# Optimization experiments

Hardware: AMD Instinct MI355X
Metric: run time of the kernel (lower is better)

Reference implementation:

```python
import jax, jax.numpy as jnp
import numpy as np

B, S, D, H = 4, 2048, 1024, 16
HD = D // H


def setup_inputs() -> dict:
    key = jax.random.key(0)
    ks = jax.random.split(key, 6)
    scale = 1.0 / np.sqrt(D)
    return {
        'x': jax.random.normal(ks[0], (B, S, D), dtype=jnp.float32),
        'wq': jax.random.normal(ks[1], (D, D), dtype=jnp.float32) * scale,
        'wk': jax.random.normal(ks[2], (D, D), dtype=jnp.float32) * scale,
        'wv': jax.random.normal(ks[3], (D, D), dtype=jnp.float32) * scale,
        'wo': jax.random.normal(ks[4], (D, D), dtype=jnp.float32) * scale,
        'wo_b': jnp.zeros((D,), dtype=jnp.float32),
    }


def reference(x, wq, wk, wv, wo, wo_b):
    b, s, _ = x.shape
    # Linear projections (torch Linear: x @ W.T), reshape to [b, h, s, hd]
    def proj(w):
        return jnp.einsum('bsd,ed->bse', x, w).reshape(b, s, H, HD).transpose(0, 2, 1, 3)
    q, k, v = proj(wq), proj(wk), proj(wv)
    scores = jnp.einsum('bhqd,bhkd->bhqk', q, k)  # [b,h,s,s]
    causal = jnp.triu(jnp.ones((s, s), dtype=bool), k=1)
    scores = jnp.where(causal, -jnp.inf, scores)
    attn = jax.nn.softmax(scores / np.sqrt(HD), axis=-1)
    ctx = jnp.einsum('bhqk,bhkd->bhqd', attn, v)  # [b,h,s,hd]
    ctx = ctx.transpose(0, 2, 1, 3).reshape(b, s, D)
    return jnp.einsum('bsd,ed->bse', ctx, wo) + wo_b
```

## Files before the change

### kernel.cpp

```cpp
#include <hip/hip_runtime.h>

#define SB 4
#define SS 2048
#define SD 1024
#define SH 16
#define SHD 64
#define SM (SB * SS)

typedef __bf16 bf16x8 __attribute__((ext_vector_type(8)));
typedef float f32x4 __attribute__((ext_vector_type(4)));

static __device__ __forceinline__ unsigned short f2bf(float x) {
    unsigned int u = __builtin_bit_cast(unsigned int, x);
    u += 0x7fffu + ((u >> 16) & 1u);
    return (unsigned short)(u >> 16);
}

static __device__ __forceinline__ float fast_exp2(float x) {
#if __has_builtin(__builtin_amdgcn_exp2f)
    return __builtin_amdgcn_exp2f(x);
#else
    return exp2f(x);
#endif
}

static __device__ __forceinline__ unsigned int pkhi(float a, float b) {
    return __builtin_amdgcn_perm(__builtin_bit_cast(unsigned int, a),
                                 __builtin_bit_cast(unsigned int, b), 0x07060302u);
}

typedef __attribute__((address_space(1))) void GV;
typedef __attribute__((address_space(3))) void LV;

static __device__ __forceinline__ void async16(const void* g, void* l) {
    __builtin_amdgcn_global_load_lds((GV*)g, (LV*)l, 16, 0, 0);
}

#define QSCALE 0.18033688011112042f

__global__ __launch_bounds__(256) void cast_all(
    const float* __restrict__ x,  const float* __restrict__ wq,
    const float* __restrict__ wk, const float* __restrict__ wv,
    const float* __restrict__ wo,
    unsigned short* __restrict__ xb, unsigned short* __restrict__ wqkv,
    unsigned short* __restrict__ wo16) {
    int i = blockIdx.x * 256 + threadIdx.x;
    const float4* src;
    ushort4* dst;
    if (i < 2097152) {
        src = reinterpret_cast<const float4*>(x) + i;
        dst = reinterpret_cast<ushort4*>(xb) + i;
    } else {
        int j = i - 2097152;
        int which = j >> 18;
        int r = j & 262143;
        const float* ws_[4] = {wq, wk, wv, wo};
        src = reinterpret_cast<const float4*>(ws_[which]) + r;
        dst = (which < 3 ? reinterpret_cast<ushort4*>(wqkv) + which * 262144
                         : reinterpret_cast<ushort4*>(wo16)) + r;
    }
    float4 v = *src;
    ushort4 o;
    o.x = f2bf(v.x); o.y = f2bf(v.y); o.z = f2bf(v.z); o.w = f2bf(v.w);
    *dst = o;
}

__device__ __forceinline__ void gemm128_mainloop(
    const unsigned short* __restrict__ A,
    const unsigned short* __restrict__ Bt,
    int Kdim, int tileM, int tileN, int tid,
    unsigned short* As, unsigned short* Bs,
    f32x4 (&acc)[4][4]) {

    const int lane = tid & 63;
    const int quad = lane >> 4;
    const int col0 = lane & 15;
    const int wr = tid >> 7;
    const int wc = (tid >> 6) & 1;

    const int srow = tid >> 2;
    const int schunk = (tid & 3) * 8;
    const unsigned short* Ab = A + (size_t)(tileM + srow) * Kdim + schunk;
    const unsigned short* Bb = Bt + (size_t)(tileN + srow) * Kdim + schunk;
    char* AsB = (char*)As + tid * 16;
    char* BsB = (char*)Bs + tid * 16;
    const size_t rowskip = (size_t)64 * Kdim;

    for (int k0 = 0; k0 < Kdim; k0 += 32) {
        __syncthreads();
        async16(Ab + k0, AsB);
        async16(Ab + k0 + rowskip, AsB + 4096);
        async16(Bb + k0, BsB);
        async16(Bb + k0 + rowskip, BsB + 4096);
        __syncthreads();

        bf16x8 af[4], bfr[4];
#pragma unroll
        for (int rt = 0; rt < 4; ++rt)
            af[rt] = *reinterpret_cast<const bf16x8*>(
                As + (wr * 64 + rt * 16 + col0) * 32 + quad * 8);
#pragma unroll
        for (int ct = 0; ct < 4; ++ct)
            bfr[ct] = *reinterpret_cast<const bf16x8*>(
                Bs + (wc * 64 + ct * 16 + col0) * 32 + quad * 8);
#pragma unroll
        for (int rt = 0; rt < 4; ++rt)
#pragma unroll
            for (int ct = 0; ct < 4; ++ct)
                acc[rt][ct] = __builtin_amdgcn_mfma_f32_16x16x32_bf16(
                    af[rt], bfr[ct], acc[rt][ct], 0, 0, 0);
    }
}

__global__ __launch_bounds__(256) void gemm_qkv(
    const unsigned short* __restrict__ xb,
    const unsigned short* __restrict__ wqkv,
    unsigned short* __restrict__ Qd,
    unsigned short* __restrict__ Kd,
    unsigned short* __restrict__ Vtd) {

    __shared__ __align__(16) unsigned short As[128 * 32];
    __shared__ __align__(16) unsigned short Bs[128 * 32];
    const int tid = threadIdx.x;
    const int tileN = blockIdx.x * 128;
    const int tileM = blockIdx.y * 128;

    f32x4 acc[4][4];
    const f32x4 z = {0.f, 0.f, 0.f, 0.f};
#pragma unroll
    for (int i = 0; i < 4; ++i)
#pragma unroll
        for (int j = 0; j < 4; ++j) acc[i][j] = z;

    gemm128_mainloop(xb, wqkv, SD, tileM, tileN, tid, As, Bs, acc);

    const int lane = tid & 63, quad = lane >> 4, col0 = lane & 15;
    const int wr = tid >> 7, wc = (tid >> 6) & 1;

#pragma unroll
    for (int ct = 0; ct < 4; ++ct) {
        int n0 = tileN + wc * 64 + ct * 16;
        int which = n0 >> 10;
        int e0 = n0 & 1023;
        int h = e0 >> 6;
        int hd = (e0 & 63) + col0;
#pragma unroll
        for (int rt = 0; rt < 4; ++rt) {
            int m0 = tileM + wr * 64 + rt * 16 + quad * 4;
            int bb = m0 >> 11;
            int s0 = m0 & 2047;
            int bh = bb * SH + h;
            if (which == 0) {
                int base = (bh * SS + s0) * SHD + hd;
#pragma unroll
                for (int r = 0; r < 4; ++r)
                    Qd[base + r * SHD] = f2bf(acc[rt][ct][r] * QSCALE);
            } else if (which == 1) {
                int base = (bh * SS + s0) * SHD + hd;
#pragma unroll
                for (int r = 0; r < 4; ++r)
                    Kd[base + r * SHD] = f2bf(acc[rt][ct][r]);
            } else {
                int base = (bh * SHD + hd) * SS + s0;
                ushort4 pk;
                pk.x = f2bf(acc[rt][ct][0]);
                pk.y = f2bf(acc[rt][ct][1]);
                pk.z = f2bf(acc[rt][ct][2]);
                pk.w = f2bf(acc[rt][ct][3]);
                *reinterpret_cast<ushort4*>(Vtd + base) = pk;
            }
        }
    }
}

__global__ __launch_bounds__(256) void gemm_out(
    const unsigned short* __restrict__ ctx,
    const unsigned short* __restrict__ wo16,
    const float* __restrict__ wb,
    float* __restrict__ out) {

    __shared__ __align__(16) unsigned short As[128 * 32];
    __shared__ __align__(16) unsigned short Bs[128 * 32];
    const int tid = threadIdx.x;
    const int tileN = blockIdx.x * 128;
    const int tileM = blockIdx.y * 128;

    f32x4 acc[4][4];
    const f32x4 z = {0.f, 0.f, 0.f, 0.f};
#pragma unroll
    for (int i = 0; i < 4; ++i)
#pragma unroll
        for (int j = 0; j < 4; ++j) acc[i][j] = z;

    gemm128_mainloop(ctx, wo16, SD, tileM, tileN, tid, As, Bs, acc);

    const int lane = tid & 63, quad = lane >> 4, col0 = lane & 15;
    const int wr = tid >> 7, wc = (tid >> 6) & 1;

#pragma unroll
    for (int ct = 0; ct < 4; ++ct) {
        int n = tileN + wc * 64 + ct * 16 + col0;
        float bias = wb[n];
#pragma unroll
        for (int rt = 0; rt < 4; ++rt) {
            int m0 = tileM + wr * 64 + rt * 16 + quad * 4;
#pragma unroll
            for (int r = 0; r < 4; ++r)
                out[(size_t)(m0 + r) * SD + n] = acc[rt][ct][r] + bias;
        }
    }
}

#define PSTR 72

__device__ __forceinline__ void attn_pass(
    const unsigned short* __restrict__ Qg,
    const unsigned short* __restrict__ Kg,
    const unsigned short* __restrict__ Vtg,
    unsigned short* __restrict__ ctx,
    size_t base, int b, int h, int jj,
    int tid, int w, int quad, int col0,
    unsigned short* Ks0, unsigned short* Ks1,
    unsigned short* Vs0, unsigned short* Vs1,
    unsigned short* Psw, const bf16x8& ones) {

    const int q0 = jj * 128 + w * 32;

    bf16x8 bq[2][2];
#pragma unroll
    for (int g = 0; g < 2; ++g)
#pragma unroll
        for (int ks = 0; ks < 2; ++ks)
            bq[g][ks] = *reinterpret_cast<const bf16x8*>(
                Qg + base + (size_t)(q0 + g * 16 + col0) * SHD + ks * 32 + quad * 8);

    f32x4 ot[2][4], lacc[2];
    const f32x4 z = {0.f, 0.f, 0.f, 0.f};
#pragma unroll
    for (int g = 0; g < 2; ++g) {
        lacc[g] = z;
#pragma unroll
        for (int ct = 0; ct < 4; ++ct) ot[g][ct] = z;
    }

    const int srow0 = tid >> 3;
    const int scs = tid & 7;

    unsigned short* KsB[2] = {Ks0, Ks1};
    unsigned short* VsB[2] = {Vs0, Vs1};

    const int nkt = 2 * jj + 2;

    __syncthreads();
#pragma unroll
    for (int j = 0; j < 2; ++j) {
        int row = j * 32 + srow0;
        int chunk = scs ^ (row & 7);
        int slot16 = (j * 256 + tid) * 16;
        async16(Kg + base + (size_t)row * SHD + chunk * 8, (char*)Ks0 + slot16);
        async16(Vtg + base + (size_t)row * SS + chunk * 8, (char*)Vs0 + slot16);
    }

    for (int kt = 0; kt < nkt; ++kt) {
        const int kb = kt * 64;
        __syncthreads();

        if (kt + 1 < nkt) {
            const int kb1 = kb + 64;
            unsigned short* Kn = KsB[(kt + 1) & 1];
            unsigned short* Vn = VsB[(kt + 1) & 1];
#pragma unroll
            for (int j = 0; j < 2; ++j) {
                int row = j * 32 + srow0;
                int chunk = scs ^ (row & 7);
                int slot16 = (j * 256 + tid) * 16;
                async16(Kg + base + (size_t)(kb1 + row) * SHD + chunk * 8,
                        (char*)Kn + slot16);
                async16(Vtg + base + (size_t)row * SS + kb1 + chunk * 8,
                        (char*)Vn + slot16);
            }
        }

        if (kb > q0 + 31) continue;

        const unsigned short* Kc = KsB[kt & 1];
        const unsigned short* Vc = VsB[kt & 1];

        bf16x8 ak[4][2];
#pragma unroll
        for (int rt = 0; rt < 4; ++rt)
#pragma unroll
            for (int ks = 0; ks < 2; ++ks)
                ak[rt][ks] = *reinterpret_cast<const bf16x8*>(
                    &Kc[(rt * 16 + col0) * 64 + ((ks * 4 + quad) ^ (col0 & 7)) * 8]);

        f32x4 sc[2][4];
#pragma unroll
        for (int g = 0; g < 2; ++g)
#pragma unroll
            for (int rt = 0; rt < 4; ++rt) sc[g][rt] = z;
#pragma unroll
        for (int rt = 0; rt < 4; ++rt)
#pragma unroll
            for (int g = 0; g < 2; ++g) {
                sc[g][rt] = __builtin_amdgcn_mfma_f32_16x16x32_bf16(
                    ak[rt][0], bq[g][0], sc[g][rt], 0, 0, 0);
                sc[g][rt] = __builtin_amdgcn_mfma_f32_16x16x32_bf16(
                    ak[rt][1], bq[g][1], sc[g][rt], 0, 0, 0);
            }

        if (kb + 63 > q0) {
#pragma unroll
            for (int g = 0; g < 2; ++g) {
                int q = q0 + g * 16 + col0;
#pragma unroll
                for (int rt = 0; rt < 4; ++rt)
#pragma unroll
                    for (int r = 0; r < 4; ++r) {
                        int key = kb + rt * 16 + quad * 4 + r;
                        if (key > q) sc[g][rt][r] = -3.0e38f;
                    }
            }
        }

#pragma unroll
        for (int g = 0; g < 2; ++g)
#pragma unroll
            for (int rt = 0; rt < 4; ++rt)
#pragma unroll
                for (int r = 0; r < 4; ++r)
                    sc[g][rt][r] = fast_exp2(sc[g][rt][r]);

#pragma unroll
        for (int g = 0; g < 2; ++g) {
            unsigned short* Pw = Psw + g * 16 * PSTR;
#pragma unroll
            for (int rt = 0; rt < 4; ++rt) {
                uint2 pk;
                pk.x = pkhi(sc[g][rt][1], sc[g][rt][0]);
                pk.y = pkhi(sc[g][rt][3], sc[g][rt][2]);
                *reinterpret_cast<uint2*>(&Pw[col0 * PSTR + rt * 16 + quad * 4]) = pk;
            }
        }

#pragma unroll
        for (int ks = 0; ks < 2; ++ks) {
            bf16x8 bp[2];
#pragma unroll
            for (int g = 0; g < 2; ++g) {
                bp[g] = *reinterpret_cast<const bf16x8*>(
                    &Psw[g * 16 * PSTR + col0 * PSTR + ks * 32 + quad * 8]);
                lacc[g] = __builtin_amdgcn_mfma_f32_16x16x32_bf16(
                    ones, bp[g], lacc[g], 0, 0, 0);
            }
#pragma unroll
            for (int ct = 0; ct < 4; ++ct) {
                bf16x8 av = *reinterpret_cast<const bf16x8*>(
                    &Vc[(ct * 16 + col0) * 64 + ((ks * 4 + quad) ^ (col0 & 7)) * 8]);
#pragma unroll
                for (int g = 0; g < 2; ++g)
                    ot[g][ct] = __builtin_amdgcn_mfma_f32_16x16x32_bf16(
                        av, bp[g], ot[g][ct], 0, 0, 0);
            }
        }
    }

#pragma unroll
    for (int g = 0; g < 2; ++g) {
        float inv = 1.0f / lacc[g][0];
        int q = q0 + g * 16 + col0;
        size_t obase = ((size_t)b * SS + q) * SD + h * SHD;
#pragma unroll
        for (int ct = 0; ct < 4; ++ct) {
            uint2 pk;
            pk.x = pkhi(ot[g][ct][1] * inv, ot[g][ct][0] * inv);
            pk.y = pkhi(ot[g][ct][3] * inv, ot[g][ct][2] * inv);
            *reinterpret_cast<uint2*>(ctx + obase + ct * 16 + quad * 4) = pk;
        }
    }
}

__global__ __launch_bounds__(256) void attn_kernel(
    const unsigned short* __restrict__ Qg,
    const unsigned short* __restrict__ Kg,
    const unsigned short* __restrict__ Vtg,
    unsigned short* __restrict__ ctx) {

    __shared__ __align__(16) unsigned short Ks0[64 * 64];
    __shared__ __align__(16) unsigned short Ks1[64 * 64];
    __shared__ __align__(16) unsigned short Vs0[64 * 64];
    __shared__ __align__(16) unsigned short Vs1[64 * 64];
    __shared__ __align__(16) unsigned short Ps[8 * 16 * PSTR];

    const int tid = threadIdx.x;
    const int w = tid >> 6;
    const int lane = tid & 63;
    const int quad = lane >> 4;
    const int col0 = lane & 15;
    const int bh = blockIdx.y;
    const int b = bh >> 4;
    const int h = bh & 15;
    const size_t base = (size_t)bh * (SS * SHD);
    unsigned short* Psw = Ps + w * 2 * 16 * PSTR;

    bf16x8 ones;
#pragma unroll
    for (int i = 0; i < 8; ++i) ones[i] = (__bf16)1.0f;

    attn_pass(Qg, Kg, Vtg, ctx, base, b, h, blockIdx.x,
              tid, w, quad, col0, Ks0, Ks1, Vs0, Vs1, Psw, ones);
    attn_pass(Qg, Kg, Vtg, ctx, base, b, h, 15 - blockIdx.x,
              tid, w, quad, col0, Ks0, Ks1, Vs0, Vs1, Psw, ones);
}

extern "C" void kernel_launch(void* const* d_in, const int* in_sizes, int n_in,
                              void* d_out, int out_size, void* d_ws, size_t ws_size,
                              hipStream_t stream) {
    const float* x  = (const float*)d_in[0];
    const float* wq = (const float*)d_in[1];
    const float* wk = (const float*)d_in[2];
    const float* wv = (const float*)d_in[3];
    const float* wo = (const float*)d_in[4];
    const float* wb = (const float*)d_in[5];
    float* out = (float*)d_out;

    char* ws = (char*)d_ws;
    unsigned short* xb   = (unsigned short*)(ws + 0);
    unsigned short* wqkv = (unsigned short*)(ws + 16777216);
    unsigned short* q    = (unsigned short*)(ws + 23068672);
    unsigned short* k    = (unsigned short*)(ws + 39845888);
    unsigned short* vt   = (unsigned short*)(ws + 56623104);
    unsigned short* ctx  = (unsigned short*)(ws + 73400320);
    unsigned short* wo16 = (unsigned short*)(ws + 90177536);

    cast_all<<<12288, 256, 0, stream>>>(x, wq, wk, wv, wo, xb, wqkv, wo16);

    gemm_qkv<<<dim3(3 * SD / 128, SM / 128), 256, 0, stream>>>(xb, wqkv, q, k, vt);

    attn_kernel<<<dim3(8, SB * SH), 256, 0, stream>>>(q, k, vt, ctx);

    gemm_out<<<dim3(SD / 128, SM / 128), 256, 0, stream>>>(ctx, wo16, wb, out);
}
```

Measured before the change: 272.5 us.

## Double-buffer GEMM shared-memory tiles and XOR-swizzle chunks to avoid bank conflicts

The shared 128x128 GEMM mainloop now ping-pongs between two LDS buffers. The next K-tile's async global-to-LDS loads are issued right after the barrier, before computing on the current tile, which drops one barrier per iteration and overlaps loads with MFMA work. The 16-byte chunk positions within each row are XOR-swizzled by row index, consistently on store and load, to reduce LDS bank conflicts on fragment reads. This doubles LDS use per block in both the QKV and output GEMMs, which may reduce occupancy.

```diff
diff --git a/kernel.cpp b/kernel.cpp
--- a/kernel.cpp
+++ b/kernel.cpp
@@ -69,7 +69,8 @@
     const unsigned short* __restrict__ A,
     const unsigned short* __restrict__ Bt,
     int Kdim, int tileM, int tileN, int tid,
-    unsigned short* As, unsigned short* Bs,
+    unsigned short* As0, unsigned short* Bs0,
+    unsigned short* As1, unsigned short* Bs1,
     f32x4 (&acc)[4][4]) {
 
     const int lane = tid & 63;
@@ -79,30 +80,51 @@
     const int wc = (tid >> 6) & 1;
 
     const int srow = tid >> 2;
-    const int schunk = (tid & 3) * 8;
+    const int schunk = ((tid & 3) ^ (srow & 3)) * 8;
     const unsigned short* Ab = A + (size_t)(tileM + srow) * Kdim + schunk;
     const unsigned short* Bb = Bt + (size_t)(tileN + srow) * Kdim + schunk;
-    char* AsB = (char*)As + tid * 16;
-    char* BsB = (char*)Bs + tid * 16;
     const size_t rowskip = (size_t)64 * Kdim;
 
-    for (int k0 = 0; k0 < Kdim; k0 += 32) {
+    unsigned short* AsB[2] = {As0, As1};
+    unsigned short* BsB[2] = {Bs0, Bs1};
+
+    const int fchunk = (quad ^ (col0 & 3)) * 8;
+    const int nkt = Kdim >> 5;
+
+    {
+        char* AsD = (char*)As0 + tid * 16;
+        char* BsD = (char*)Bs0 + tid * 16;
+        async16(Ab, AsD);
+        async16(Ab + rowskip, AsD + 4096);
+        async16(Bb, BsD);
+        async16(Bb + rowskip, BsD + 4096);
+    }
+
+    for (int kt = 0; kt < nkt; ++kt) {
         __syncthreads();
-        async16(Ab + k0, AsB);
-        async16(Ab + k0 + rowskip, AsB + 4096);
-        async16(Bb + k0, BsB);
-        async16(Bb + k0 + rowskip, BsB + 4096);
-        __syncthreads();
+
+        if (kt + 1 < nkt) {
+            int k0 = (kt + 1) << 5;
+            char* AsD = (char*)AsB[(kt + 1) & 1] + tid * 16;
+            char* BsD = (char*)BsB[(kt + 1) & 1] + tid * 16;
+            async16(Ab + k0, AsD);
+            async16(Ab + k0 + rowskip, AsD + 4096);
+            async16(Bb + k0, BsD);
+            async16(Bb + k0 + rowskip, BsD + 4096);
+        }
+
+        const unsigned short* Asc = AsB[kt & 1];
+        const unsigned short* Bsc = BsB[kt & 1];
 
         bf16x8 af[4], bfr[4];
 #pragma unroll
         for (int rt = 0; rt < 4; ++rt)
             af[rt] = *reinterpret_cast<const bf16x8*>(
-                As + (wr * 64 + rt * 16 + col0) * 32 + quad * 8);
+                Asc + (wr * 64 + rt * 16 + col0) * 32 + fchunk);
 #pragma unroll
         for (int ct = 0; ct < 4; ++ct)
             bfr[ct] = *reinterpret_cast<const bf16x8*>(
-                Bs + (wc * 64 + ct * 16 + col0) * 32 + quad * 8);
+                Bsc + (wc * 64 + ct * 16 + col0) * 32 + fchunk);
 #pragma unroll
         for (int rt = 0; rt < 4; ++rt)
 #pragma unroll
@@ -119,8 +141,10 @@
     unsigned short* __restrict__ Kd,
     unsigned short* __restrict__ Vtd) {
 
-    __shared__ __align__(16) unsigned short As[128 * 32];
-    __shared__ __align__(16) unsigned short Bs[128 * 32];
+    __shared__ __align__(16) unsigned short As0[128 * 32];
+    __shared__ __align__(16) unsigned short Bs0[128 * 32];
+    __shared__ __align__(16) unsigned short As1[128 * 32];
+    __shared__ __align__(16) unsigned short Bs1[128 * 32];
     const int tid = threadIdx.x;
     const int tileN = blockIdx.x * 128;
     const int tileM = blockIdx.y * 128;
@@ -132,7 +156,7 @@
 #pragma unroll
         for (int j = 0; j < 4; ++j) acc[i][j] = z;
 
-    gemm128_mainloop(xb, wqkv, SD, tileM, tileN, tid, As, Bs, acc);
+    gemm128_mainloop(xb, wqkv, SD, tileM, tileN, tid, As0, Bs0, As1, Bs1, acc);
 
     const int lane = tid & 63, quad = lane >> 4, col0 = lane & 15;
     const int wr = tid >> 7, wc = (tid >> 6) & 1;
@@ -179,8 +203,10 @@
     const float* __restrict__ wb,
     float* __restrict__ out) {
 
-    __shared__ __align__(16) unsigned short As[128 * 32];
-    __shared__ __align__(16) unsigned short Bs[128 * 32];
+    __shared__ __align__(16) unsigned short As0[128 * 32];
+    __shared__ __align__(16) unsigned short Bs0[128 * 32];
+    __shared__ __align__(16) unsigned short As1[128 * 32];
+    __shared__ __align__(16) unsigned short Bs1[128 * 32];
     const int tid = threadIdx.x;
     const int tileN = blockIdx.x * 128;
     const int tileM = blockIdx.y * 128;
@@ -192,7 +218,7 @@
 #pragma unroll
         for (int j = 0; j < 4; ++j) acc[i][j] = z;
 
-    gemm128_mainloop(ctx, wo16, SD, tileM, tileN, tid, As, Bs, acc);
+    gemm128_mainloop(ctx, wo16, SD, tileM, tileN, tid, As0, Bs0, As1, Bs1, acc);
 
     const int lane = tid & 63, quad = lane >> 4, col0 = lane & 15;
     const int wr = tid >> 7, wc = (tid >> 6) & 1;
```

Result: slower. 296.0 us (+8.6%).
